# Kernel optimization log

Measured on AMD Instinct MI355X. Metric: run time of the kernel, lower is better.

Reference implementation:

```python
import jax, jax.numpy as jnp
import numpy as np

DIM, D_STATE, D_CONV, EXPAND = 512, 16, 4, 2
D_INNER = EXPAND * DIM            # 1024
DT_RANK = (DIM + 15) // 16        # 32
B, L = 2, 2048


def setup_inputs() -> dict:
    key = jax.random.key(0)
    ks = jax.random.split(key, 12)
    s_in = 1.0 / np.sqrt(DIM)
    s_xp = 1.0 / np.sqrt(D_INNER)
    s_dt = 1.0 / np.sqrt(DT_RANK)
    return {
        "x": jax.random.normal(ks[0], (B, L, DIM), jnp.float32),
        "ln_g": jnp.ones((DIM,), jnp.float32),
        "ln_b": jnp.zeros((DIM,), jnp.float32),
        "W_in": jax.random.normal(ks[1], (2 * D_INNER, DIM), jnp.float32) * s_in,
        "conv_w": jax.random.normal(ks[2], (D_INNER, D_CONV), jnp.float32) * 0.5,
        "conv_b": jax.random.normal(ks[3], (D_INNER,), jnp.float32) * 0.1,
        "W_xproj": jax.random.normal(ks[4], (DT_RANK + 2 * D_STATE, D_INNER), jnp.float32) * s_xp,
        "W_dt": jax.random.normal(ks[5], (D_INNER, DT_RANK), jnp.float32) * s_dt,
        "b_dt": jax.random.normal(ks[6], (D_INNER,), jnp.float32) * 0.1 - 4.0,  # softplus -> small dt
        "A_log": jnp.log(jax.random.uniform(ks[7], (D_INNER, D_STATE), jnp.float32, 1.0, 16.0)),
        "Dp": jax.random.normal(ks[8], (D_INNER,), jnp.float32),
        "W_out": jax.random.normal(ks[9], (DIM, D_INNER), jnp.float32) * s_xp,
    }


def _layernorm(x, g, b, eps=1e-5):
    mu = jnp.mean(x, -1, keepdims=True)
    var = jnp.mean(jnp.square(x - mu), -1, keepdims=True)
    return (x - mu) * jax.lax.rsqrt(var + eps) * g + b


def reference(x, ln_g, ln_b, W_in, conv_w, conv_b, W_xproj, W_dt, b_dt, A_log, Dp, W_out):
    h = _layernorm(x, ln_g, ln_b)
    # input projection -> [B,L,2*d_inner]
    xz = jnp.einsum('bld,ed->ble', h, W_in)
    xp, z = jnp.split(xz, 2, axis=-1)
    # depthwise causal conv1d over time (kernel d_conv), then SiLU
    xp_pad = jnp.pad(xp, ((0, 0), (D_CONV - 1, 0), (0, 0)))
    xc = conv_b
    for k in range(D_CONV):
        xc = xc + xp_pad[:, k:k + L, :] * conv_w[:, k]
    xc = jax.nn.silu(xc)
    # x_proj -> dt, B, C
    proj = jnp.einsum('bld,ed->ble', xc, W_xproj)
    dt_r = proj[..., :DT_RANK]
    Bm = proj[..., DT_RANK:DT_RANK + D_STATE]          # [B,L,n]
    Cm = proj[..., DT_RANK + D_STATE:]                 # [B,L,n]
    dt = jax.nn.softplus(jnp.einsum('blr,dr->bld', dt_r, W_dt) + b_dt)  # [B,L,d]
    A = -jnp.exp(A_log)                                # [d,n]
    dA = jnp.exp(jnp.einsum('bld,dn->bldn', dt, A))    # [B,L,d,n]
    dBx = dt[..., None] * Bm[:, :, None, :] * xc[..., None]  # [B,L,d,n]
    # selective scan over time (time-major for lax.scan)
    def step(s, inp):
        dA_t, dBx_t, C_t = inp
        s = s * dA_t + dBx_t                           # [B,d,n]
        y_t = jnp.einsum('bdn,bn->bd', s, C_t)
        return s, y_t
    s0 = jnp.zeros((B, D_INNER, D_STATE), xc.dtype)
    _, ys = jax.lax.scan(step, s0,
                         (jnp.moveaxis(dA, 1, 0), jnp.moveaxis(dBx, 1, 0), jnp.moveaxis(Cm, 1, 0)))
    y = jnp.moveaxis(ys, 0, 1)                         # [B,L,d]
    y = y + xc * Dp
    y = y * jax.nn.silu(z)
    out = jnp.einsum('bld,ed->ble', y, W_out)
    return x + out  # dropout is identity in eval mode
```

## Files before the change

### kernel.cpp

```cpp
#include <hip/hip_runtime.h>
#include <hip/hip_bf16.h>
#include <math.h>

#define B_      2
#define L_      2048
#define DIM_    512
#define DINNER  1024
#define DTRANK  32
#define DSTATE  16
#define DCONV   4
#define BL      (B_ * L_)
#define NCHUNK  64
#define CLEN    (L_ / NCHUNK)

typedef __attribute__((ext_vector_type(8))) short bf16x8;
typedef __attribute__((ext_vector_type(4))) float f32x4;

static __device__ __forceinline__ unsigned short f2bf(float f) {
  __hip_bfloat16 h = __float2bfloat16(f);
  return *(unsigned short*)&h;
}
static __device__ __forceinline__ float bf2f(unsigned short u) {
  return __uint_as_float(((unsigned int)u) << 16);
}

static __device__ __forceinline__ void gload16(const void* g, void* l) {
  __builtin_amdgcn_global_load_lds(
      (const __attribute__((address_space(1))) void*)g,
      (__attribute__((address_space(3))) void*)l, 16, 0, 0);
}

static __device__ __forceinline__ float softplus_f(float acc) {
  return (acc > 20.f) ? acc : __logf(1.f + __expf(acc));
}

__global__ __launch_bounds__(256) void cvt_ln_kernel(
    const float* __restrict__ s0, const float* __restrict__ s1,
    const float* __restrict__ s2, __hip_bfloat16* __restrict__ d0,
    __hip_bfloat16* __restrict__ d1, __hip_bfloat16* __restrict__ d2,
    const float* __restrict__ x, const float* __restrict__ g,
    const float* __restrict__ b, __hip_bfloat16* __restrict__ h) {
  int blk = blockIdx.x;
  if (blk < 1600) {
    int i = (blk * 256 + threadIdx.x) * 4;
    const float* s; __hip_bfloat16* d; int off;
    if (i < 1048576)            { s = s0; d = d0; off = i; }
    else if (i < 1048576+65536) { s = s1; d = d1; off = i - 1048576; }
    else                        { s = s2; d = d2; off = i - 1114112; }
    float4 v = *(const float4*)(s + off);
    d[off + 0] = __float2bfloat16(v.x);
    d[off + 1] = __float2bfloat16(v.y);
    d[off + 2] = __float2bfloat16(v.z);
    d[off + 3] = __float2bfloat16(v.w);
    return;
  }
  int row = (blk - 1600) * 4 + (threadIdx.x >> 6);
  int lane = threadIdx.x & 63;
  const float* xr = x + (size_t)row * DIM_;
  float v[8];
  float sum = 0.f;
#pragma unroll
  for (int i = 0; i < 8; i++) { v[i] = xr[lane + i * 64]; sum += v[i]; }
#pragma unroll
  for (int o = 32; o > 0; o >>= 1) sum += __shfl_xor(sum, o, 64);
  float mu = sum * (1.f / DIM_);
  float vs = 0.f;
#pragma unroll
  for (int i = 0; i < 8; i++) { float dd = v[i] - mu; vs += dd * dd; }
#pragma unroll
  for (int o = 32; o > 0; o >>= 1) vs += __shfl_xor(vs, o, 64);
  float rstd = rsqrtf(vs * (1.f / DIM_) + 1e-5f);
  __hip_bfloat16* hr = h + (size_t)row * DIM_;
#pragma unroll
  for (int i = 0; i < 8; i++) {
    int c = lane + i * 64;
    hr[c] = __float2bfloat16((v[i] - mu) * rstd * g[c] + b[c]);
  }
}

template <bool ADD_RES, bool OUT_BF16>
__global__ __launch_bounds__(256) void gemm_mfma_128(
    const __hip_bfloat16* __restrict__ A, int lda,
    const __hip_bfloat16* __restrict__ Bw, int ldb,
    const float* __restrict__ Res, int ldr,
    void* __restrict__ C, int ldc, int K) {
  __shared__ short As[128 * 64];
  __shared__ short Bs[128 * 64];
  int t = threadIdx.x;
  int n0 = blockIdx.x * 128, m0 = blockIdx.y * 128;
  int w = t >> 6, lane = t & 63;
  int wm = (w >> 1) * 64, wn = (w & 1) * 64;
  int l15 = lane & 15, quad = lane >> 4;
  int lr = lane >> 3, lc = (lane & 7) * 8;
  const short* Ag = (const short*)A + (size_t)(m0 + w * 32 + lr) * lda + lc;
  const short* Bg = (const short*)Bw + (size_t)(n0 + w * 32 + lr) * ldb + lc;
  f32x4 acc[4][4];
#pragma unroll
  for (int i = 0; i < 4; i++)
#pragma unroll
    for (int j = 0; j < 4; j++) acc[i][j] = (f32x4){0.f, 0.f, 0.f, 0.f};
  for (int k0 = 0; k0 < K; k0 += 64) {
    __syncthreads();
#pragma unroll
    for (int p = 0; p < 4; p++) {
      gload16(Ag + (size_t)(p * 8) * lda + k0, &As[(w * 32 + p * 8) * 64]);
      gload16(Bg + (size_t)(p * 8) * ldb + k0, &Bs[(w * 32 + p * 8) * 64]);
    }
    __syncthreads();
#pragma unroll
    for (int kk = 0; kk < 64; kk += 32) {
      bf16x8 af[4], bfr[4];
#pragma unroll
      for (int i = 0; i < 4; i++) {
        af[i] = *(const bf16x8*)&As[(wm + i * 16 + l15) * 64 + kk + quad * 8];
        bfr[i] = *(const bf16x8*)&Bs[(wn + i * 16 + l15) * 64 + kk + quad * 8];
      }
#pragma unroll
      for (int i = 0; i < 4; i++)
#pragma unroll
        for (int j = 0; j < 4; j++)
          acc[i][j] = __builtin_amdgcn_mfma_f32_16x16x32_bf16(
              af[i], bfr[j], acc[i][j], 0, 0, 0);
    }
  }
#pragma unroll
  for (int i = 0; i < 4; i++)
#pragma unroll
    for (int r = 0; r < 4; r++) {
      int row = m0 + wm + i * 16 + quad * 4 + r;
#pragma unroll
      for (int j = 0; j < 4; j++) {
        int col = n0 + wn + j * 16 + l15;
        float v = acc[i][j][r];
        if (ADD_RES) v += Res[(size_t)row * ldr + col];
        if (OUT_BF16)
          ((unsigned short*)C)[(size_t)row * ldc + col] = f2bf(v);
        else
          ((float*)C)[(size_t)row * ldc + col] = v;
      }
    }
}

template <bool ADD_RES>
__global__ __launch_bounds__(256) void gemm_mfma_64(
    const __hip_bfloat16* __restrict__ A, int lda,
    const __hip_bfloat16* __restrict__ Bw, int ldb,
    const float* __restrict__ Res, int ldr,
    float* __restrict__ C, int ldc, int K, size_t czs) {
  __shared__ short As[64 * 64];
  __shared__ short Bs[64 * 64];
  int t = threadIdx.x;
  int n0 = blockIdx.x * 64, m0 = blockIdx.y * 64;
  size_t kbase = (size_t)blockIdx.z * K;
  int w = t >> 6, lane = t & 63;
  int wm = (w >> 1) * 32, wn = (w & 1) * 32;
  int l15 = lane & 15, quad = lane >> 4;
  int lr = lane >> 3, lc = (lane & 7) * 8;
  const short* Ag = (const short*)A + (size_t)(m0 + w * 16 + lr) * lda + lc + kbase;
  const short* Bg = (const short*)Bw + (size_t)(n0 + w * 16 + lr) * ldb + lc + kbase;
  f32x4 acc[2][2];
#pragma unroll
  for (int i = 0; i < 2; i++)
#pragma unroll
    for (int j = 0; j < 2; j++) acc[i][j] = (f32x4){0.f, 0.f, 0.f, 0.f};
  for (int k0 = 0; k0 < K; k0 += 64) {
    __syncthreads();
#pragma unroll
    for (int p = 0; p < 2; p++) {
      gload16(Ag + (size_t)(p * 8) * lda + k0, &As[(w * 16 + p * 8) * 64]);
      gload16(Bg + (size_t)(p * 8) * ldb + k0, &Bs[(w * 16 + p * 8) * 64]);
    }
    __syncthreads();
#pragma unroll
    for (int kk = 0; kk < 64; kk += 32) {
      bf16x8 af[2], bfr[2];
#pragma unroll
      for (int i = 0; i < 2; i++) {
        af[i] = *(const bf16x8*)&As[(wm + i * 16 + l15) * 64 + kk + quad * 8];
        bfr[i] = *(const bf16x8*)&Bs[(wn + i * 16 + l15) * 64 + kk + quad * 8];
      }
#pragma unroll
      for (int i = 0; i < 2; i++)
#pragma unroll
        for (int j = 0; j < 2; j++)
          acc[i][j] = __builtin_amdgcn_mfma_f32_16x16x32_bf16(
              af[i], bfr[j], acc[i][j], 0, 0, 0);
    }
  }
  float* Cz = C + czs * blockIdx.z;
#pragma unroll
  for (int i = 0; i < 2; i++)
#pragma unroll
    for (int r = 0; r < 4; r++) {
      int row = m0 + wm + i * 16 + quad * 4 + r;
#pragma unroll
      for (int j = 0; j < 2; j++) {
        int col = n0 + wn + j * 16 + l15;
        float v = acc[i][j][r];
        if (ADD_RES) v += Res[(size_t)row * ldr + col];
        Cz[(size_t)row * ldc + col] = v;
      }
    }
}

__global__ __launch_bounds__(256) void conv_silu_kernel(
    const unsigned short* __restrict__ xzb, const float* __restrict__ cw,
    const float* __restrict__ cb, __hip_bfloat16* __restrict__ xc_bf) {
  int idx = blockIdx.x * 256 + threadIdx.x;
  int d4 = (idx & 255) * 4;
  int bl = idx >> 8;
  int l = bl & (L_ - 1);
  const unsigned short* base = xzb + (size_t)bl * 2048 + d4;
  float4 acc = *(const float4*)(cb + d4);
  float4 w0 = *(const float4*)(cw + (d4 + 0) * 4);
  float4 w1 = *(const float4*)(cw + (d4 + 1) * 4);
  float4 w2 = *(const float4*)(cw + (d4 + 2) * 4);
  float4 w3 = *(const float4*)(cw + (d4 + 3) * 4);
  if (l >= 3) {
    ushort4 r = *(const ushort4*)(base - 3 * 2048);
    acc.x += bf2f(r.x) * w0.x; acc.y += bf2f(r.y) * w1.x;
    acc.z += bf2f(r.z) * w2.x; acc.w += bf2f(r.w) * w3.x;
  }
  if (l >= 2) {
    ushort4 r = *(const ushort4*)(base - 2 * 2048);
    acc.x += bf2f(r.x) * w0.y; acc.y += bf2f(r.y) * w1.y;
    acc.z += bf2f(r.z) * w2.y; acc.w += bf2f(r.w) * w3.y;
  }
  if (l >= 1) {
    ushort4 r = *(const ushort4*)(base - 1 * 2048);
    acc.x += bf2f(r.x) * w0.z; acc.y += bf2f(r.y) * w1.z;
    acc.z += bf2f(r.z) * w2.z; acc.w += bf2f(r.w) * w3.z;
  }
  {
    ushort4 r = *(const ushort4*)(base);
    acc.x += bf2f(r.x) * w0.w; acc.y += bf2f(r.y) * w1.w;
    acc.z += bf2f(r.z) * w2.w; acc.w += bf2f(r.w) * w3.w;
  }
  float4 v;
  v.x = acc.x / (1.f + __expf(-acc.x));
  v.y = acc.y / (1.f + __expf(-acc.y));
  v.z = acc.z / (1.f + __expf(-acc.z));
  v.w = acc.w / (1.f + __expf(-acc.w));
  ushort4 hb;
  hb.x = f2bf(v.x); hb.y = f2bf(v.y); hb.z = f2bf(v.z); hb.w = f2bf(v.w);
  *(ushort4*)(xc_bf + (size_t)bl * DINNER + d4) = hb;
}

__global__ __launch_bounds__(256) void dt_kernel(
    const float* __restrict__ pp, float* __restrict__ proj,
    const float* __restrict__ Wdt, const float* __restrict__ bdt,
    float* __restrict__ dt) {
  int blk = blockIdx.x;
  int dgrp = blk & 3;
  int bl0 = (blk >> 2) * 8;
  int tid = threadIdx.x;
  int d = dgrp * 256 + tid;
  __shared__ float pr[8 * 64];
  float w[32];
#pragma unroll
  for (int q = 0; q < 8; q++) {
    float4 wv = *(const float4*)(Wdt + (size_t)d * 32 + q * 4);
    w[q * 4 + 0] = wv.x; w[q * 4 + 1] = wv.y;
    w[q * 4 + 2] = wv.z; w[q * 4 + 3] = wv.w;
  }
  float bias = bdt[d];
  if (tid < 128) {
    int o4 = bl0 * 16 + tid;
    float4 v0 = ((const float4*)pp)[o4];
    float4 v1 = ((const float4*)pp)[o4 + 65536];
    float4 v2 = ((const float4*)pp)[o4 + 131072];
    float4 v3 = ((const float4*)pp)[o4 + 196608];
    float4 s;
    s.x = (v0.x + v1.x) + (v2.x + v3.x);
    s.y = (v0.y + v1.y) + (v2.y + v3.y);
    s.z = (v0.z + v1.z) + (v2.z + v3.z);
    s.w = (v0.w + v1.w) + (v2.w + v3.w);
    ((float4*)pr)[tid] = s;
    if (dgrp == 0) *(float4*)(proj + (size_t)bl0 * 64 + tid * 4) = s;
  }
  __syncthreads();
#pragma unroll
  for (int row = 0; row < 8; row++) {
    float a0 = 0.f, a1 = 0.f, a2 = 0.f, a3 = 0.f;
#pragma unroll
    for (int q = 0; q < 8; q++) {
      float4 pv = *(const float4*)&pr[row * 64 + q * 4];
      a0 = fmaf(pv.x, w[q * 4 + 0], a0);
      a1 = fmaf(pv.y, w[q * 4 + 1], a1);
      a2 = fmaf(pv.z, w[q * 4 + 2], a2);
      a3 = fmaf(pv.w, w[q * 4 + 3], a3);
    }
    float acc = bias + ((a0 + a1) + (a2 + a3));
    dt[(size_t)(bl0 + row) * DINNER + d] = softplus_f(acc);
  }
}

__global__ __launch_bounds__(256) void scan1_kernel(
    const float* __restrict__ dt, const __hip_bfloat16* __restrict__ xc_bf,
    const float* __restrict__ proj, const float* __restrict__ A_log,
    float* __restrict__ T, float* __restrict__ E) {
  int bid = blockIdx.x;
  int dgrp = bid & 63;
  int c = (bid >> 6) & (NCHUNK - 1);
  int b = bid >> 12;
  int tid = threadIdx.x;
  int n = tid & 15;
  int dl = tid >> 4;
  int d = dgrp * 16 + dl;
  int l0 = c * CLEN;
  __shared__ float dts[CLEN * 16];
  __shared__ float dxs[CLEN * 16];
  __shared__ float Bsh[CLEN * 16];
  for (int i = tid; i < CLEN * 16; i += 256) {
    int row = i >> 4, col = i & 15;
    size_t bl = (size_t)(b * L_ + l0 + row);
    float dtv = dt[bl * DINNER + dgrp * 16 + col];
    float xv = __bfloat162float(xc_bf[bl * DINNER + dgrp * 16 + col]);
    dts[i] = dtv;
    dxs[i] = dtv * xv;
    Bsh[i] = proj[bl * 64 + 32 + col];
  }
  float Aa = -__expf(A_log[(size_t)d * 16 + n]);
  __syncthreads();
  float Tn = 1.f, En = 0.f;
#pragma unroll 8
  for (int l = 0; l < CLEN; l++) {
    float dA = __expf(dts[l * 16 + dl] * Aa);
    Tn *= dA;
    En = En * dA + dxs[l * 16 + dl] * Bsh[l * 16 + n];
  }
  size_t o = (((size_t)b * NCHUNK + c) * DINNER + d) * 16 + n;
  T[o] = Tn; E[o] = En;
}

__global__ __launch_bounds__(256) void combine_kernel(
    float* __restrict__ T, const float* __restrict__ E) {
  int idx = blockIdx.x * 256 + threadIdx.x;
  int b = idx >> 14;
  int dn = idx & 16383;
  size_t base = (size_t)b * NCHUNK * (DINNER * 16) + dn;
  float s = 0.f;
#pragma unroll
  for (int batch = 0; batch < 4; batch++) {
    float t[16], e[16];
#pragma unroll
    for (int j = 0; j < 16; j++) {
      size_t o = base + (size_t)(batch * 16 + j) * (DINNER * 16);
      t[j] = T[o]; e[j] = E[o];
    }
#pragma unroll
    for (int j = 0; j < 16; j++) {
      T[base + (size_t)(batch * 16 + j) * (DINNER * 16)] = s;
      s = t[j] * s + e[j];
    }
  }
}

__global__ __launch_bounds__(256) void scan2_kernel(
    const float* __restrict__ dt, const __hip_bfloat16* __restrict__ xc_bf,
    const float* __restrict__ proj, const float* __restrict__ A_log,
    const float* __restrict__ Sstart, const float* __restrict__ Dp,
    unsigned short* __restrict__ xzb) {
  int bid = blockIdx.x;
  int dgrp = bid & 3;
  int c = (bid >> 2) & (NCHUNK - 1);
  int b = bid >> 8;
  int d = dgrp * 256 + threadIdx.x;
  int l0 = c * CLEN;
  __shared__ float Bs[CLEN * 16];
  __shared__ float Cs[CLEN * 16];
  for (int i = threadIdx.x; i < CLEN * 16; i += 256) {
    int row = i >> 4, nn = i & 15;
    const float* pr = proj + (size_t)(b * L_ + l0 + row) * 64;
    Bs[i] = pr[32 + nn];
    Cs[i] = pr[48 + nn];
  }
  float Aa[16], s[16];
  size_t sb = (((size_t)b * NCHUNK + c) * DINNER + d) * 16;
#pragma unroll
  for (int q = 0; q < 4; q++) {
    float4 av = *(const float4*)(A_log + (size_t)d * 16 + q * 4);
    Aa[q * 4 + 0] = -__expf(av.x); Aa[q * 4 + 1] = -__expf(av.y);
    Aa[q * 4 + 2] = -__expf(av.z); Aa[q * 4 + 3] = -__expf(av.w);
    float4 sv = *(const float4*)(Sstart + sb + q * 4);
    s[q * 4 + 0] = sv.x; s[q * 4 + 1] = sv.y;
    s[q * 4 + 2] = sv.z; s[q * 4 + 3] = sv.w;
  }
  float Dv = Dp[d];
  __syncthreads();
  for (int l = l0; l < l0 + CLEN; l++) {
    int bl = b * L_ + l;
    float dtv = dt[(size_t)bl * DINNER + d];
    float xv = __bfloat162float(xc_bf[(size_t)bl * DINNER + d]);
    float dx = dtv * xv;
    int lrow = (l - l0) * 16;
    float y = 0.f;
#pragma unroll
    for (int n = 0; n < 16; n++) {
      float dA = __expf(dtv * Aa[n]);
      s[n] = s[n] * dA + dx * Bs[lrow + n];
      y += s[n] * Cs[lrow + n];
    }
    float zv = bf2f(xzb[(size_t)bl * 2048 + 1024 + d]);
    float gate = zv / (1.f + __expf(-zv));
    xzb[(size_t)bl * 2048 + d] = f2bf((y + xv * Dv) * gate);
  }
}

extern "C" void kernel_launch(void* const* d_in, const int* in_sizes, int n_in,
                              void* d_out, int out_size, void* d_ws, size_t ws_size,
                              hipStream_t stream) {
  const float* x      = (const float*)d_in[0];
  const float* ln_g   = (const float*)d_in[1];
  const float* ln_b   = (const float*)d_in[2];
  const float* W_in   = (const float*)d_in[3];
  const float* conv_w = (const float*)d_in[4];
  const float* conv_b = (const float*)d_in[5];
  const float* W_xprj = (const float*)d_in[6];
  const float* W_dt   = (const float*)d_in[7];
  const float* b_dt   = (const float*)d_in[8];
  const float* A_log  = (const float*)d_in[9];
  const float* Dp     = (const float*)d_in[10];
  const float* W_out  = (const float*)d_in[11];
  float* out = (float*)d_out;

  float* ws     = (float*)d_ws;
  float* xzb_f  = ws;
  float* xcbf_f = xzb_f + 4194304;
  float* proj   = xcbf_f + 2097152;
  float* pp     = proj + 262144;
  float* dtb    = pp + 1048576;
  float* T      = dtb + 4194304;
  float* E      = T + 2097152;
  float* hbf_f  = E + 2097152;
  float* wbf    = hbf_f + 1048576;

  unsigned short* xzb   = (unsigned short*)xzb_f;
  __hip_bfloat16* xc_bf = (__hip_bfloat16*)xcbf_f;
  __hip_bfloat16* h_bf  = (__hip_bfloat16*)hbf_f;
  __hip_bfloat16* Wb_in = (__hip_bfloat16*)wbf;
  __hip_bfloat16* Wb_xp = Wb_in + 1048576;
  __hip_bfloat16* Wb_out = Wb_xp + 65536;
  __hip_bfloat16* y_bf  = (__hip_bfloat16*)xzb;

  cvt_ln_kernel<<<1600 + BL / 4, 256, 0, stream>>>(
      W_in, W_xprj, W_out, Wb_in, Wb_xp, Wb_out, x, ln_g, ln_b, h_bf);
  gemm_mfma_128<false, true><<<dim3(2 * DINNER / 128, BL / 128), 256, 0, stream>>>(
      h_bf, DIM_, Wb_in, DIM_, nullptr, 0, xzb, 2 * DINNER, DIM_);
  conv_silu_kernel<<<(BL * DINNER / 4) / 256, 256, 0, stream>>>(
      xzb, conv_w, conv_b, xc_bf);
  gemm_mfma_64<false><<<dim3(1, BL / 64, 4), 256, 0, stream>>>(
      xc_bf, DINNER, Wb_xp, DINNER, nullptr, 0, pp, 64, 256, 262144);
  dt_kernel<<<(BL / 8) * 4, 256, 0, stream>>>(pp, proj, W_dt, b_dt, dtb);
  scan1_kernel<<<B_ * NCHUNK * 64, 256, 0, stream>>>(dtb, xc_bf, proj, A_log, T, E);
  combine_kernel<<<(B_ * DINNER * 16) / 256, 256, 0, stream>>>(T, E);
  scan2_kernel<<<B_ * NCHUNK * 4, 256, 0, stream>>>(dtb, xc_bf, proj, A_log, T, Dp, xzb);
  gemm_mfma_64<true><<<dim3(DIM_ / 64, BL / 64, 1), 256, 0, stream>>>(
      y_bf, 2048, Wb_out, DINNER, x, DIM_, out, DIM_, DINNER, 0);
}
```

Before: 213.0 us.

## Fuse causal conv+SiLU into x_proj GEMM A-tile load; prefetch scan2 inputs

The depthwise causal conv and SiLU are now computed while staging the A tile of the x_proj GEMM. Each block convolves its own rows and K-slice, writes the bf16 result to shared memory for the MFMA and to global memory for later kernels. This removes one kernel launch and a read of xc_bf before the GEMM, at the cost of more work per block during the A load. Separately, scan2 now preloads all dt, x and z values for its chunk into registers before the sequential loop. That raises register pressure in exchange for taking global load latency off the serial recurrence.

New measurement: 190.9 us. 1.12x faster.

```diff
diff --git a/kernel.cpp b/kernel.cpp
--- a/kernel.cpp
+++ b/kernel.cpp
@@ -203,47 +203,101 @@
     }
 }
 
-__global__ __launch_bounds__(256) void conv_silu_kernel(
-    const unsigned short* __restrict__ xzb, const float* __restrict__ cw,
-    const float* __restrict__ cb, __hip_bfloat16* __restrict__ xc_bf) {
-  int idx = blockIdx.x * 256 + threadIdx.x;
-  int d4 = (idx & 255) * 4;
-  int bl = idx >> 8;
+__global__ __launch_bounds__(256) void gemm_proj_conv(
+    const unsigned short* __restrict__ xzb,
+    const __hip_bfloat16* __restrict__ Bw,
+    const float* __restrict__ cw, const float* __restrict__ cb,
+    __hip_bfloat16* __restrict__ xc_bf,
+    float* __restrict__ C, size_t czs) {
+  __shared__ short As[64 * 64];
+  __shared__ short Bs[64 * 64];
+  __shared__ float cws[256 * 4];
+  __shared__ float cbs[256];
+  int t = threadIdx.x;
+  int m0 = blockIdx.y * 64;
+  int kbase = blockIdx.z * 256;
+  int w = t >> 6, lane = t & 63;
+  int wm = (w >> 1) * 32, wn = (w & 1) * 32;
+  int l15 = lane & 15, quad = lane >> 4;
+  int lrB = lane >> 3, lcB = (lane & 7) * 8;
+  const short* Bg = (const short*)Bw + (size_t)(w * 16 + lrB) * DINNER + lcB + kbase;
+  *(float4*)&cws[t * 4] = *(const float4*)(cw + (size_t)(kbase + t) * 4);
+  cbs[t] = cb[kbase + t];
+  int ar = t >> 2, aq = t & 3;
+  int bl = m0 + ar;
   int l = bl & (L_ - 1);
-  const unsigned short* base = xzb + (size_t)bl * 2048 + d4;
-  float4 acc = *(const float4*)(cb + d4);
-  float4 w0 = *(const float4*)(cw + (d4 + 0) * 4);
-  float4 w1 = *(const float4*)(cw + (d4 + 1) * 4);
-  float4 w2 = *(const float4*)(cw + (d4 + 2) * 4);
-  float4 w3 = *(const float4*)(cw + (d4 + 3) * 4);
-  if (l >= 3) {
-    ushort4 r = *(const ushort4*)(base - 3 * 2048);
-    acc.x += bf2f(r.x) * w0.x; acc.y += bf2f(r.y) * w1.x;
-    acc.z += bf2f(r.z) * w2.x; acc.w += bf2f(r.w) * w3.x;
-  }
-  if (l >= 2) {
-    ushort4 r = *(const ushort4*)(base - 2 * 2048);
-    acc.x += bf2f(r.x) * w0.y; acc.y += bf2f(r.y) * w1.y;
-    acc.z += bf2f(r.z) * w2.y; acc.w += bf2f(r.w) * w3.y;
-  }
-  if (l >= 1) {
-    ushort4 r = *(const ushort4*)(base - 1 * 2048);
-    acc.x += bf2f(r.x) * w0.z; acc.y += bf2f(r.y) * w1.z;
-    acc.z += bf2f(r.z) * w2.z; acc.w += bf2f(r.w) * w3.z;
-  }
-  {
-    ushort4 r = *(const ushort4*)(base);
-    acc.x += bf2f(r.x) * w0.w; acc.y += bf2f(r.y) * w1.w;
-    acc.z += bf2f(r.z) * w2.w; acc.w += bf2f(r.w) * w3.w;
-  }
-  float4 v;
-  v.x = acc.x / (1.f + __expf(-acc.x));
-  v.y = acc.y / (1.f + __expf(-acc.y));
-  v.z = acc.z / (1.f + __expf(-acc.z));
-  v.w = acc.w / (1.f + __expf(-acc.w));
-  ushort4 hb;
-  hb.x = f2bf(v.x); hb.y = f2bf(v.y); hb.z = f2bf(v.z); hb.w = f2bf(v.w);
-  *(ushort4*)(xc_bf + (size_t)bl * DINNER + d4) = hb;
+  f32x4 acc[2][2];
+#pragma unroll
+  for (int i = 0; i < 2; i++)
+#pragma unroll
+    for (int j = 0; j < 2; j++) acc[i][j] = (f32x4){0.f, 0.f, 0.f, 0.f};
+  for (int k0 = 0; k0 < 256; k0 += 64) {
+    __syncthreads();
+#pragma unroll
+    for (int p = 0; p < 2; p++)
+      gload16(Bg + k0 + (size_t)(p * 8) * DINNER, &Bs[(w * 16 + p * 8) * 64]);
+    int dl0 = k0 + aq * 16;
+    const unsigned short* xrow = xzb + (size_t)bl * 2048 + kbase + dl0;
+    float o[16];
+#pragma unroll
+    for (int cc = 0; cc < 16; cc++) o[cc] = cbs[dl0 + cc];
+#pragma unroll
+    for (int k = 0; k < 4; k++) {
+      int off = 3 - k;
+      bool ok = (l >= off);
+      const unsigned short* src = xrow - (size_t)(ok ? off : 0) * 2048;
+      bf16x8 v0 = *(const bf16x8*)(src);
+      bf16x8 v1 = *(const bf16x8*)(src + 8);
+#pragma unroll
+      for (int cc = 0; cc < 8; cc++) {
+        float xa = ok ? bf2f((unsigned short)v0[cc]) : 0.f;
+        float xb = ok ? bf2f((unsigned short)v1[cc]) : 0.f;
+        o[cc]     = fmaf(xa, cws[(dl0 + cc) * 4 + k], o[cc]);
+        o[cc + 8] = fmaf(xb, cws[(dl0 + cc + 8) * 4 + k], o[cc + 8]);
+      }
+    }
+    bf16x8 pa, pb;
+#pragma unroll
+    for (int cc = 0; cc < 8; cc++) {
+      float va = o[cc] / (1.f + __expf(-o[cc]));
+      float vb = o[cc + 8] / (1.f + __expf(-o[cc + 8]));
+      pa[cc] = (short)f2bf(va);
+      pb[cc] = (short)f2bf(vb);
+    }
+    *(bf16x8*)&As[ar * 64 + aq * 16] = pa;
+    *(bf16x8*)&As[ar * 64 + aq * 16 + 8] = pb;
+    unsigned short* xcd = (unsigned short*)xc_bf + (size_t)bl * DINNER + kbase + dl0;
+    *(bf16x8*)xcd = pa;
+    *(bf16x8*)(xcd + 8) = pb;
+    __syncthreads();
+#pragma unroll
+    for (int kk = 0; kk < 64; kk += 32) {
+      bf16x8 af[2], bfr[2];
+#pragma unroll
+      for (int i = 0; i < 2; i++) {
+        af[i] = *(const bf16x8*)&As[(wm + i * 16 + l15) * 64 + kk + quad * 8];
+        bfr[i] = *(const bf16x8*)&Bs[(wn + i * 16 + l15) * 64 + kk + quad * 8];
+      }
+#pragma unroll
+      for (int i = 0; i < 2; i++)
+#pragma unroll
+        for (int j = 0; j < 2; j++)
+          acc[i][j] = __builtin_amdgcn_mfma_f32_16x16x32_bf16(
+              af[i], bfr[j], acc[i][j], 0, 0, 0);
+    }
+  }
+  float* Cz = C + czs * blockIdx.z;
+#pragma unroll
+  for (int i = 0; i < 2; i++)
+#pragma unroll
+    for (int r = 0; r < 4; r++) {
+      int row = m0 + wm + i * 16 + quad * 4 + r;
+#pragma unroll
+      for (int j = 0; j < 2; j++) {
+        int col = wn + j * 16 + l15;
+        Cz[(size_t)row * 64 + col] = acc[i][j][r];
+      }
+    }
 }
 
 __global__ __launch_bounds__(256) void dt_kernel(
@@ -365,15 +419,25 @@
   int dgrp = bid & 3;
   int c = (bid >> 2) & (NCHUNK - 1);
   int b = bid >> 8;
-  int d = dgrp * 256 + threadIdx.x;
+  int tid = threadIdx.x;
+  int d = dgrp * 256 + tid;
   int l0 = c * CLEN;
-  __shared__ float Bs[CLEN * 16];
-  __shared__ float Cs[CLEN * 16];
-  for (int i = threadIdx.x; i < CLEN * 16; i += 256) {
+  __shared__ float Bsh[CLEN * 16];
+  __shared__ float Csh[CLEN * 16];
+  for (int i = tid; i < CLEN * 16; i += 256) {
     int row = i >> 4, nn = i & 15;
     const float* pr = proj + (size_t)(b * L_ + l0 + row) * 64;
-    Bs[i] = pr[32 + nn];
-    Cs[i] = pr[48 + nn];
+    Bsh[i] = pr[32 + nn];
+    Csh[i] = pr[48 + nn];
+  }
+  float dtr[CLEN], xvr[CLEN];
+  unsigned short zr[CLEN];
+#pragma unroll
+  for (int l = 0; l < CLEN; l++) {
+    size_t bl = (size_t)(b * L_ + l0 + l);
+    dtr[l] = dt[bl * DINNER + d];
+    xvr[l] = __bfloat162float(xc_bf[bl * DINNER + d]);
+    zr[l] = xzb[bl * 2048 + 1024 + d];
   }
   float Aa[16], s[16];
   size_t sb = (((size_t)b * NCHUNK + c) * DINNER + d) * 16;
@@ -388,22 +452,21 @@
   }
   float Dv = Dp[d];
   __syncthreads();
-  for (int l = l0; l < l0 + CLEN; l++) {
-    int bl = b * L_ + l;
-    float dtv = dt[(size_t)bl * DINNER + d];
-    float xv = __bfloat162float(xc_bf[(size_t)bl * DINNER + d]);
+#pragma unroll
+  for (int l = 0; l < CLEN; l++) {
+    float dtv = dtr[l];
+    float xv = xvr[l];
     float dx = dtv * xv;
-    int lrow = (l - l0) * 16;
     float y = 0.f;
 #pragma unroll
     for (int n = 0; n < 16; n++) {
       float dA = __expf(dtv * Aa[n]);
-      s[n] = s[n] * dA + dx * Bs[lrow + n];
-      y += s[n] * Cs[lrow + n];
-    }
-    float zv = bf2f(xzb[(size_t)bl * 2048 + 1024 + d]);
+      s[n] = s[n] * dA + dx * Bsh[l * 16 + n];
+      y += s[n] * Csh[l * 16 + n];
+    }
+    float zv = bf2f(zr[l]);
     float gate = zv / (1.f + __expf(-zv));
-    xzb[(size_t)bl * 2048 + d] = f2bf((y + xv * Dv) * gate);
+    xzb[(size_t)(b * L_ + l0 + l) * 2048 + d] = f2bf((y + xv * Dv) * gate);
   }
 }
 
@@ -447,10 +510,8 @@
       W_in, W_xprj, W_out, Wb_in, Wb_xp, Wb_out, x, ln_g, ln_b, h_bf);
   gemm_mfma_128<false, true><<<dim3(2 * DINNER / 128, BL / 128), 256, 0, stream>>>(
       h_bf, DIM_, Wb_in, DIM_, nullptr, 0, xzb, 2 * DINNER, DIM_);
-  conv_silu_kernel<<<(BL * DINNER / 4) / 256, 256, 0, stream>>>(
-      xzb, conv_w, conv_b, xc_bf);
-  gemm_mfma_64<false><<<dim3(1, BL / 64, 4), 256, 0, stream>>>(
-      xc_bf, DINNER, Wb_xp, DINNER, nullptr, 0, pp, 64, 256, 262144);
+  gemm_proj_conv<<<dim3(1, BL / 64, 4), 256, 0, stream>>>(
+      xzb, Wb_xp, conv_w, conv_b, xc_bf, pp, 262144);
   dt_kernel<<<(BL / 8) * 4, 256, 0, stream>>>(pp, proj, W_dt, b_dt, dtb);
   scan1_kernel<<<B_ * NCHUNK * 64, 256, 0, stream>>>(dtb, xc_bf, proj, A_log, T, E);
   combine_kernel<<<(B_ * DINNER * 16) / 256, 256, 0, stream>>>(T, E);
```
